# Kernel tuning notes

Hardware: AMD Instinct MI355X
Metric: run time of the kernel (lower is better)

## Reference

```python
import jax, jax.numpy as jnp
import numpy as np

DIM = 1024
HEADS = 16
HEAD_DIM = DIM // HEADS
N = 4096
EPS = 1e-5


def setup_inputs() -> dict:
    key = jax.random.key(0)
    ks = jax.random.split(key, 12)
    s = DIM ** -0.5  # init scale for weights
    return {
        "z1": jax.random.normal(ks[0], (N, DIM), jnp.float32),
        "z2": jax.random.normal(ks[1], (N, DIM), jnp.float32),
        "wq": jax.random.normal(ks[2], (DIM, DIM), jnp.float32) * s,
        "bq": jax.random.normal(ks[3], (DIM,), jnp.float32) * 0.01,
        "wk": jax.random.normal(ks[4], (DIM, DIM), jnp.float32) * s,
        "bk": jax.random.normal(ks[5], (DIM,), jnp.float32) * 0.01,
        "wv1": jax.random.normal(ks[6], (DIM, DIM), jnp.float32) * s,
        "bv1": jax.random.normal(ks[7], (DIM,), jnp.float32) * 0.01,
        "wv2": jax.random.normal(ks[8], (DIM, DIM), jnp.float32) * s,
        "bv2": jax.random.normal(ks[9], (DIM,), jnp.float32) * 0.01,
        "g1": jnp.ones((DIM,), jnp.float32),
        "be1": jnp.zeros((DIM,), jnp.float32),
        "g2": jnp.ones((DIM,), jnp.float32),
        "be2": jnp.zeros((DIM,), jnp.float32),
    }


def _layernorm(x, g, b):
    mu = jnp.mean(x, axis=-1, keepdims=True)
    var = jnp.mean(jnp.square(x - mu), axis=-1, keepdims=True)
    return (x - mu) * jax.lax.rsqrt(var + EPS) * g + b


def _split_heads(x):  # [n, dim] -> [h, n, c]
    n = x.shape[0]
    return x.reshape(n, HEADS, HEAD_DIM).swapaxes(0, 1)


def reference(z1, z2, wq, bq, wk, bk, wv1, bv1, wv2, bv2, g1, be1, g2, be2):
    scale = DIM ** -0.5
    n1 = _layernorm(z1, g1, be1)
    n2 = _layernorm(z2, g2, be2)
    q = _split_heads(n1 @ wq.T + bq)    # [h, n, c]
    k = _split_heads(n2 @ wk.T + bk)    # [h, m, c]
    v = _split_heads(n2 @ wv1.T + bv1)  # [h, m, c]
    v1 = _split_heads(n1 @ wv2.T + bv2) # [h, n, c]
    sim = jnp.einsum('hnc,hmc->hnm', q, k) * scale
    attn = jax.nn.softmax(sim, axis=-1)                       # [h, n, m]
    z_c = jnp.einsum('hnm,hmc->hnc', attn, v)                 # attn @ v
    c_z = jnp.einsum('hnm,hnc->hmc', attn, v1)                # attn.T @ v1
    z_c = z_c.swapaxes(0, 1).reshape(z1.shape[0], DIM)
    c_z = c_z.swapaxes(0, 1).reshape(z2.shape[0], DIM)
    # torch's attn.squeeze(0) is a no-op for HEADS > 1
    return z_c, c_z, attn
```

## Files before the change

kernel.cpp:

```cpp
#include <hip/hip_runtime.h>

#define NN 4096
#define DIM 1024
#define HEADS 16
#define HD 64
#define SCALE 0.03125f

typedef __attribute__((ext_vector_type(8))) short bf16x8;
typedef __attribute__((ext_vector_type(4))) short short4v;
typedef __attribute__((ext_vector_type(4))) float f32x4;
typedef __attribute__((ext_vector_type(4))) unsigned int u32x4;

__device__ __forceinline__ short f2bf(float f) {
  unsigned int x = __float_as_uint(f);
  unsigned int r = x + 0x7FFFu + ((x >> 16) & 1u);
  return (short)(r >> 16);
}
__device__ __forceinline__ unsigned int cvtpk(float a, float b) {
  unsigned int r;
  asm("v_cvt_pk_bf16_f32 %0, %1, %2" : "=v"(r) : "v"(a), "v"(b));
  return r;
}

#define GLL16(gp, lp) __builtin_amdgcn_global_load_lds( \
    (const __attribute__((address_space(1))) unsigned int*)(gp), \
    (__attribute__((address_space(3))) unsigned int*)(lp), 16, 0, 0)

#define MFMA16(a, b, c) __builtin_amdgcn_mfma_f32_16x16x32_bf16(a, b, c, 0, 0, 0)

__global__ __launch_bounds__(256) void ln_kernel(
    const float* __restrict__ z1, const float* __restrict__ z2,
    const float* __restrict__ g1, const float* __restrict__ be1,
    const float* __restrict__ g2, const float* __restrict__ be2,
    short* __restrict__ n1, short* __restrict__ n2) {
  int row = blockIdx.x;
  int which = blockIdx.y;
  const float* src = (which ? z2 : z1) + (size_t)row * DIM;
  const float* g  = which ? g2 : g1;
  const float* be = which ? be2 : be1;
  short* dst = (which ? n2 : n1) + (size_t)row * DIM;
  int t = threadIdx.x;
  float4 v = ((const float4*)src)[t];
  float s  = v.x + v.y + v.z + v.w;
  float s2 = v.x*v.x + v.y*v.y + v.z*v.z + v.w*v.w;
#pragma unroll
  for (int off = 32; off >= 1; off >>= 1) {
    s  += __shfl_xor(s, off);
    s2 += __shfl_xor(s2, off);
  }
  __shared__ __align__(16) float ls[8];
  int wid = t >> 6;
  if ((t & 63) == 0) { ls[wid] = s; ls[wid + 4] = s2; }
  __syncthreads();
  s  = ls[0] + ls[1] + ls[2] + ls[3];
  s2 = ls[4] + ls[5] + ls[6] + ls[7];
  float mu = s * (1.0f / DIM);
  float var = s2 * (1.0f / DIM) - mu * mu;
  float rs = rsqrtf(var + 1e-5f);
  float4 gv = ((const float4*)g)[t];
  float4 bv = ((const float4*)be)[t];
  short4v o;
  o.x = f2bf((v.x - mu) * rs * gv.x + bv.x);
  o.y = f2bf((v.y - mu) * rs * gv.y + bv.y);
  o.z = f2bf((v.z - mu) * rs * gv.z + bv.z);
  o.w = f2bf((v.w - mu) * rs * gv.w + bv.w);
  ((short4v*)dst)[t] = o;
}

__global__ __launch_bounds__(256) void cvt_w_kernel(
    const float* __restrict__ w0, const float* __restrict__ w1,
    const float* __restrict__ w2, const float* __restrict__ w3,
    short* __restrict__ wb) {
  int y = blockIdx.y;
  const float* src = (y == 0) ? w0 : (y == 1) ? w1 : (y == 2) ? w2 : w3;
  size_t i = (size_t)blockIdx.x * 256 + threadIdx.x;
  float4 v = ((const float4*)src)[i];
  short4v o;
  o.x = f2bf(v.x); o.y = f2bf(v.y); o.z = f2bf(v.z); o.w = f2bf(v.w);
  ((short4v*)(wb + (size_t)y * DIM * DIM))[i] = o;
}

__global__ __launch_bounds__(256) void proj_kernel(
    const short* __restrict__ n1, const short* __restrict__ n2,
    const short* __restrict__ wb,
    const float* __restrict__ bq, const float* __restrict__ bk,
    const float* __restrict__ bv1, const float* __restrict__ bv2,
    short* __restrict__ q, short* __restrict__ k,
    short* __restrict__ vT, short* __restrict__ v1T) {
  int z = blockIdx.z;
  const short* A = (z == 1 || z == 2) ? n2 : n1;
  const short* B = wb + (size_t)z * DIM * DIM;
  const float* bias = (z == 0) ? bq : (z == 1) ? bk : (z == 2) ? bv1 : bv2;
  int i0 = blockIdx.y * 128, j0 = blockIdx.x * 128;
  __shared__ __align__(16) short As[128 * 32];
  __shared__ __align__(16) short Bs[128 * 32];
  int t = threadIdx.x;
  int wid = t >> 6, lane = t & 63, g = lane >> 4, l15 = lane & 15;
  int wi = (wid >> 1) * 64, wj = (wid & 1) * 64;
  f32x4 acc[4][4] = {};
  for (int kt = 0; kt < DIM; kt += 32) {
    __syncthreads();
#pragma unroll
    for (int e = 0; e < 2; ++e) {
      int lin = e * 256 + t;
      int row = lin >> 2, kc = (lin & 3) * 8;
      GLL16(A + (size_t)(i0 + row) * DIM + kt + kc, As + lin * 8);
      GLL16(B + (size_t)(j0 + row) * DIM + kt + kc, Bs + lin * 8);
    }
    __syncthreads();
    bf16x8 af[4], bfr[4];
#pragma unroll
    for (int it = 0; it < 4; ++it)
      af[it] = *(const bf16x8*)(As + (wi + it * 16 + l15) * 32 + g * 8);
#pragma unroll
    for (int jt = 0; jt < 4; ++jt)
      bfr[jt] = *(const bf16x8*)(Bs + (wj + jt * 16 + l15) * 32 + g * 8);
#pragma unroll
    for (int it = 0; it < 4; ++it)
#pragma unroll
      for (int jt = 0; jt < 4; ++jt)
        acc[it][jt] = MFMA16(af[it], bfr[jt], acc[it][jt]);
  }
  if (z < 2) {
    short* out = (z == 0) ? q : k;
#pragma unroll
    for (int jt = 0; jt < 4; ++jt) {
      int j = j0 + wj + jt * 16 + l15;
      float bj = bias[j];
#pragma unroll
      for (int it = 0; it < 4; ++it) {
        int i = i0 + wi + it * 16 + g * 4;
#pragma unroll
        for (int r = 0; r < 4; ++r)
          out[(size_t)(i + r) * DIM + j] = f2bf(acc[it][jt][r] + bj);
      }
    }
  } else {
    short* out = (z == 2) ? vT : v1T;
#pragma unroll
    for (int jt = 0; jt < 4; ++jt) {
      int j = j0 + wj + jt * 16 + l15;
      float bj = bias[j];
#pragma unroll
      for (int it = 0; it < 4; ++it) {
        int i = i0 + wi + it * 16 + g * 4;
        short4v o;
#pragma unroll
        for (int r = 0; r < 4; ++r) o[r] = f2bf(acc[it][jt][r] + bj);
        *(short4v*)(out + (size_t)j * NN + i) = o;
      }
    }
  }
}

__global__ __launch_bounds__(256, 4) void p2zc_kernel(
    const short* __restrict__ q, const short* __restrict__ k,
    const short* __restrict__ vT, float* __restrict__ attn,
    float* __restrict__ zc, float* __restrict__ iSx) {
  int bid = (int)(blockIdx.y * gridDim.x + blockIdx.x);
  int vid = (bid & 7) * 128 + (bid >> 3);
  int h = vid >> 6;
  int nblk = vid & 63;
  int t = threadIdx.x, wid = t >> 6, lane = t & 63;
  int g = lane >> 4, l15 = lane & 15;
  int nw = nblk * 64 + wid * 16;

  const short* qp = q + (size_t)(nw + l15) * DIM + h * HD + g * 8;
  bf16x8 qb0 = *(const bf16x8*)(qp);
  bf16x8 qb1 = *(const bf16x8*)(qp + 32);

  __shared__ __align__(16) short Ks[128 * 64];
  __shared__ __align__(16) short Vs[64 * 128];
  const short* kb = k + h * HD;
  const short* vb = vT + (size_t)h * HD * NN;

  f32x4 Sp = {0.f, 0.f, 0.f, 0.f};
  for (int mc = 0; mc < NN; mc += 128) {
    __syncthreads();
#pragma unroll
    for (int e = 0; e < 4; ++e) {
      int L = e * 256 + t, row = L >> 3, c = L & 7;
      GLL16(kb + (size_t)(mc + row) * DIM + ((c ^ (row & 7)) * 8), Ks + L * 8);
    }
    __syncthreads();
#pragma unroll
    for (int mt = 0; mt < 8; ++mt) {
      const short* kr = Ks + (mt * 16 + l15) * 64;
      bf16x8 ka0 = *(const bf16x8*)(kr + ((g ^ (l15 & 7)) * 8));
      bf16x8 ka1 = *(const bf16x8*)(kr + (((g + 4) ^ (l15 & 7)) * 8));
      f32x4 acc = {0.f, 0.f, 0.f, 0.f};
      acc = MFMA16(ka0, qb0, acc);
      acc = MFMA16(ka1, qb1, acc);
#pragma unroll
      for (int r = 0; r < 4; ++r) Sp[r] += __expf(acc[r] * SCALE);
    }
  }
  float S = Sp[0] + Sp[1] + Sp[2] + Sp[3];
  S += __shfl_xor(S, 16);
  S += __shfl_xor(S, 32);
  float iS = 1.0f / S;
  if (lane < 16) iSx[h * NN + nw + l15] = iS;

  float* ab = attn + (size_t)h * NN * NN;
  f32x4 azc[4] = {};
  for (int mc = 0; mc < NN; mc += 128) {
    __syncthreads();
#pragma unroll
    for (int e = 0; e < 4; ++e) {
      int L = e * 256 + t, row = L >> 3, c = L & 7;
      GLL16(kb + (size_t)(mc + row) * DIM + ((c ^ (row & 7)) * 8), Ks + L * 8);
    }
#pragma unroll
    for (int e = 0; e < 4; ++e) {
      int L = e * 256 + t, row = L >> 4, c = L & 15;
      GLL16(vb + (size_t)row * NN + mc + ((c ^ (row & 15)) * 8), Vs + L * 8);
    }
    __syncthreads();
    float p[8][4];
#pragma unroll
    for (int mt = 0; mt < 8; ++mt) {
      const short* kr = Ks + (mt * 16 + l15) * 64;
      bf16x8 ka0 = *(const bf16x8*)(kr + ((g ^ (l15 & 7)) * 8));
      bf16x8 ka1 = *(const bf16x8*)(kr + (((g + 4) ^ (l15 & 7)) * 8));
      f32x4 acc = {0.f, 0.f, 0.f, 0.f};
      acc = MFMA16(ka0, qb0, acc);
      acc = MFMA16(ka1, qb1, acc);
      f32x4 pv;
#pragma unroll
      for (int r = 0; r < 4; ++r) { pv[r] = __expf(acc[r] * SCALE) * iS; p[mt][r] = pv[r]; }
      *(f32x4*)(ab + (size_t)(nw + l15) * NN + mc + mt * 16 + g * 4) = pv;
    }
#pragma unroll
    for (int km = 0; km < 4; ++km) {
      unsigned int a0p = cvtpk(p[2*km][0],   p[2*km][1]);
      unsigned int a1p = cvtpk(p[2*km][2],   p[2*km][3]);
      unsigned int b0p = cvtpk(p[2*km+1][0], p[2*km+1][1]);
      unsigned int b1p = cvtpk(p[2*km+1][2], p[2*km+1][3]);
      int s0 = ((g & 1) * 2) * 16 + l15, s1 = s0 + 16;
      bool hi = g >= 2;
      unsigned int w0a = __shfl(a0p, s0), w0b = __shfl(b0p, s0);
      unsigned int w1a = __shfl(a1p, s0), w1b = __shfl(b1p, s0);
      unsigned int w2a = __shfl(a0p, s1), w2b = __shfl(b0p, s1);
      unsigned int w3a = __shfl(a1p, s1), w3b = __shfl(b1p, s1);
      union { u32x4 u; bf16x8 s; } pw;
      pw.u[0] = hi ? w0b : w0a; pw.u[1] = hi ? w1b : w1a;
      pw.u[2] = hi ? w2b : w2a; pw.u[3] = hi ? w3b : w3a;
#pragma unroll
      for (int ct = 0; ct < 4; ++ct) {
        bf16x8 pb = *(const bf16x8*)(Vs + (ct * 16 + l15) * 128 + (((km * 4 + g) ^ l15) * 8));
        azc[ct] = MFMA16(pw.s, pb, azc[ct]);
      }
    }
  }
#pragma unroll
  for (int ct = 0; ct < 4; ++ct)
#pragma unroll
    for (int r = 0; r < 4; ++r)
      zc[(size_t)(nw + g * 4 + r) * DIM + h * HD + ct * 16 + l15] = azc[ct][r];
}

__global__ __launch_bounds__(256, 4) void czr_kernel(
    const short* __restrict__ q, const short* __restrict__ k,
    const short* __restrict__ v1T, const float* __restrict__ iSx,
    float* __restrict__ cz) {
  int bid = (int)(blockIdx.y * gridDim.x + blockIdx.x);
  int vid = (bid & 7) * 128 + (bid >> 3);
  int h = vid >> 6;
  int mblk = vid & 63;
  int t = threadIdx.x, wid = t >> 6, lane = t & 63;
  int g = lane >> 4, l15 = lane & 15;
  int mw = mblk * 64 + wid * 16;

  const short* kp = k + (size_t)(mw + l15) * DIM + h * HD + g * 8;
  bf16x8 kb0 = *(const bf16x8*)(kp);
  bf16x8 kb1 = *(const bf16x8*)(kp + 32);

  __shared__ __align__(16) short Qs[128 * 64];
  __shared__ __align__(16) short V1s[64 * 128];
  const short* qb = q + h * HD;
  const short* vb = v1T + (size_t)h * HD * NN;
  const float* iSb = iSx + h * NN;

  f32x4 acz[4] = {};
  for (int nc = 0; nc < NN; nc += 128) {
    __syncthreads();
#pragma unroll
    for (int e = 0; e < 4; ++e) {
      int L = e * 256 + t, row = L >> 3, c = L & 7;
      GLL16(qb + (size_t)(nc + row) * DIM + ((c ^ (row & 7)) * 8), Qs + L * 8);
    }
#pragma unroll
    for (int e = 0; e < 4; ++e) {
      int L = e * 256 + t, row = L >> 4, c = L & 15;
      GLL16(vb + (size_t)row * NN + nc + ((c ^ (row & 15)) * 8), V1s + L * 8);
    }
    __syncthreads();
    float p[8][4];
#pragma unroll
    for (int nt = 0; nt < 8; ++nt) {
      const short* qr = Qs + (nt * 16 + l15) * 64;
      bf16x8 qa0 = *(const bf16x8*)(qr + ((g ^ (l15 & 7)) * 8));
      bf16x8 qa1 = *(const bf16x8*)(qr + (((g + 4) ^ (l15 & 7)) * 8));
      f32x4 acc = {0.f, 0.f, 0.f, 0.f};
      acc = MFMA16(qa0, kb0, acc);
      acc = MFMA16(qa1, kb1, acc);
      f32x4 is4 = *(const f32x4*)(iSb + nc + nt * 16 + g * 4);
#pragma unroll
      for (int r = 0; r < 4; ++r) p[nt][r] = __expf(acc[r] * SCALE) * is4[r];
    }
#pragma unroll
    for (int kn = 0; kn < 4; ++kn) {
      unsigned int a0p = cvtpk(p[2*kn][0],   p[2*kn][1]);
      unsigned int a1p = cvtpk(p[2*kn][2],   p[2*kn][3]);
      unsigned int b0p = cvtpk(p[2*kn+1][0], p[2*kn+1][1]);
      unsigned int b1p = cvtpk(p[2*kn+1][2], p[2*kn+1][3]);
      int s0 = ((g & 1) * 2) * 16 + l15, s1 = s0 + 16;
      bool hi = g >= 2;
      unsigned int w0a = __shfl(a0p, s0), w0b = __shfl(b0p, s0);
      unsigned int w1a = __shfl(a1p, s0), w1b = __shfl(b1p, s0);
      unsigned int w2a = __shfl(a0p, s1), w2b = __shfl(b0p, s1);
      unsigned int w3a = __shfl(a1p, s1), w3b = __shfl(b1p, s1);
      union { u32x4 u; bf16x8 s; } pw;
      pw.u[0] = hi ? w0b : w0a; pw.u[1] = hi ? w1b : w1a;
      pw.u[2] = hi ? w2b : w2a; pw.u[3] = hi ? w3b : w3a;
#pragma unroll
      for (int ct = 0; ct < 4; ++ct) {
        bf16x8 pb = *(const bf16x8*)(V1s + (ct * 16 + l15) * 128 + (((kn * 4 + g) ^ l15) * 8));
        acz[ct] = MFMA16(pw.s, pb, acz[ct]);
      }
    }
  }
#pragma unroll
  for (int ct = 0; ct < 4; ++ct)
#pragma unroll
    for (int r = 0; r < 4; ++r)
      cz[(size_t)(mw + g * 4 + r) * DIM + h * HD + ct * 16 + l15] = acz[ct][r];
}

extern "C" void kernel_launch(void* const* d_in, const int* in_sizes, int n_in,
                              void* d_out, int out_size, void* d_ws, size_t ws_size,
                              hipStream_t stream) {
  static const int expect[14] = {4194304, 4194304, 1048576, 1024, 1048576, 1024,
                                 1048576, 1024, 1048576, 1024, 1024, 1024, 1024, 1024};
  if (n_in != 14) return;
  for (int i = 0; i < 14; ++i) if (in_sizes[i] != expect[i]) return;
  if (out_size != 2 * NN * DIM + (size_t)HEADS * NN * NN) return;

  const float* z1  = (const float*)d_in[0];
  const float* z2  = (const float*)d_in[1];
  const float* wq  = (const float*)d_in[2];
  const float* bq  = (const float*)d_in[3];
  const float* wk  = (const float*)d_in[4];
  const float* bk  = (const float*)d_in[5];
  const float* wv1 = (const float*)d_in[6];
  const float* bv1 = (const float*)d_in[7];
  const float* wv2 = (const float*)d_in[8];
  const float* bv2 = (const float*)d_in[9];
  const float* g1  = (const float*)d_in[10];
  const float* be1 = (const float*)d_in[11];
  const float* g2  = (const float*)d_in[12];
  const float* be2 = (const float*)d_in[13];

  float* out  = (float*)d_out;
  float* zc   = out;
  float* cz   = out + (size_t)NN * DIM;
  float* attn = out + 2 * (size_t)NN * DIM;

  short* n1 = (short*)zc;
  short* n2 = (short*)cz;
  short* wb = (short*)attn;

  char* ws = (char*)d_ws;
  const size_t MB = 1024 * 1024;
  short* q   = (short*)(ws);
  short* k   = (short*)(ws + 8 * MB);
  short* vT  = (short*)(ws + 16 * MB);
  short* v1T = (short*)(ws + 24 * MB);
  float* iSx = (float*)(ws + 32 * MB);

  ln_kernel<<<dim3(NN, 2), 256, 0, stream>>>(z1, z2, g1, be1, g2, be2, n1, n2);
  cvt_w_kernel<<<dim3(DIM * DIM / 1024, 4), 256, 0, stream>>>(wq, wk, wv1, wv2, wb);
  proj_kernel<<<dim3(DIM / 128, NN / 128, 4), 256, 0, stream>>>(n1, n2, wb, bq, bk, bv1, bv2, q, k, vT, v1T);
  p2zc_kernel<<<dim3(NN / 64, HEADS), 256, 0, stream>>>(q, k, vT, attn, zc, iSx);
  czr_kernel<<<dim3(NN / 64, HEADS), 256, 0, stream>>>(q, k, v1T, iSx, cz);
}
```

Before: 559.0 us.

## Double per-wave row tiles, use native exp2, prescale v1 by inverse row sums

Each wave now handles two 16-row tiles in the attention kernels, so each K/Q tile loaded into LDS is reused twice as often and the grid is halved. __expf is replaced by a raw v_exp_f32 on a prescaled argument. A new small kernel folds the per-row inverse softmax sums into v1T beforehand, which removes the iSx loads and multiplies from the czr inner loop. The cost is more registers and accumulators per wave, which may reduce occupancy, and a small extra bf16 rounding step on v1.

```diff
diff --git a/kernel.cpp b/kernel.cpp
--- a/kernel.cpp
+++ b/kernel.cpp
@@ -5,6 +5,7 @@
 #define HEADS 16
 #define HD 64
 #define SCALE 0.03125f
+#define EXP2S 0.04508422002778011f
 
 typedef __attribute__((ext_vector_type(8))) short bf16x8;
 typedef __attribute__((ext_vector_type(4))) short short4v;
@@ -16,9 +17,17 @@
   unsigned int r = x + 0x7FFFu + ((x >> 16) & 1u);
   return (short)(r >> 16);
 }
+__device__ __forceinline__ float bf2f(short s) {
+  return __uint_as_float(((unsigned int)(unsigned short)s) << 16);
+}
 __device__ __forceinline__ unsigned int cvtpk(float a, float b) {
   unsigned int r;
   asm("v_cvt_pk_bf16_f32 %0, %1, %2" : "=v"(r) : "v"(a), "v"(b));
+  return r;
+}
+__device__ __forceinline__ float exp2x(float x) {
+  float r;
+  asm("v_exp_f32 %0, %1" : "=v"(r) : "v"(x));
   return r;
 }
 
@@ -158,23 +167,27 @@
     const short* __restrict__ vT, float* __restrict__ attn,
     float* __restrict__ zc, float* __restrict__ iSx) {
   int bid = (int)(blockIdx.y * gridDim.x + blockIdx.x);
-  int vid = (bid & 7) * 128 + (bid >> 3);
-  int h = vid >> 6;
-  int nblk = vid & 63;
+  int vid = (bid & 7) * 64 + (bid >> 3);
+  int h = vid >> 5;
+  int base = (vid & 31) * 128;
   int t = threadIdx.x, wid = t >> 6, lane = t & 63;
   int g = lane >> 4, l15 = lane & 15;
-  int nw = nblk * 64 + wid * 16;
-
-  const short* qp = q + (size_t)(nw + l15) * DIM + h * HD + g * 8;
-  bf16x8 qb0 = *(const bf16x8*)(qp);
-  bf16x8 qb1 = *(const bf16x8*)(qp + 32);
+  int nw[2] = {base + wid * 16, base + 64 + wid * 16};
+
+  bf16x8 qb[2][2];
+#pragma unroll
+  for (int tl = 0; tl < 2; ++tl) {
+    const short* qp = q + (size_t)(nw[tl] + l15) * DIM + h * HD + g * 8;
+    qb[tl][0] = *(const bf16x8*)(qp);
+    qb[tl][1] = *(const bf16x8*)(qp + 32);
+  }
 
   __shared__ __align__(16) short Ks[128 * 64];
   __shared__ __align__(16) short Vs[64 * 128];
   const short* kb = k + h * HD;
   const short* vb = vT + (size_t)h * HD * NN;
 
-  f32x4 Sp = {0.f, 0.f, 0.f, 0.f};
+  float Sp[2][4] = {};
   for (int mc = 0; mc < NN; mc += 128) {
     __syncthreads();
 #pragma unroll
@@ -188,21 +201,28 @@
       const short* kr = Ks + (mt * 16 + l15) * 64;
       bf16x8 ka0 = *(const bf16x8*)(kr + ((g ^ (l15 & 7)) * 8));
       bf16x8 ka1 = *(const bf16x8*)(kr + (((g + 4) ^ (l15 & 7)) * 8));
-      f32x4 acc = {0.f, 0.f, 0.f, 0.f};
-      acc = MFMA16(ka0, qb0, acc);
-      acc = MFMA16(ka1, qb1, acc);
-#pragma unroll
-      for (int r = 0; r < 4; ++r) Sp[r] += __expf(acc[r] * SCALE);
-    }
-  }
-  float S = Sp[0] + Sp[1] + Sp[2] + Sp[3];
-  S += __shfl_xor(S, 16);
-  S += __shfl_xor(S, 32);
-  float iS = 1.0f / S;
-  if (lane < 16) iSx[h * NN + nw + l15] = iS;
+#pragma unroll
+      for (int tl = 0; tl < 2; ++tl) {
+        f32x4 acc = {0.f, 0.f, 0.f, 0.f};
+        acc = MFMA16(ka0, qb[tl][0], acc);
+        acc = MFMA16(ka1, qb[tl][1], acc);
+#pragma unroll
+        for (int r = 0; r < 4; ++r) Sp[tl][r] += exp2x(acc[r] * EXP2S);
+      }
+    }
+  }
+  float iS[2];
+#pragma unroll
+  for (int tl = 0; tl < 2; ++tl) {
+    float S = Sp[tl][0] + Sp[tl][1] + Sp[tl][2] + Sp[tl][3];
+    S += __shfl_xor(S, 16);
+    S += __shfl_xor(S, 32);
+    iS[tl] = 1.0f / S;
+    if (lane < 16) iSx[h * NN + nw[tl] + l15] = iS[tl];
+  }
 
   float* ab = attn + (size_t)h * NN * NN;
-  f32x4 azc[4] = {};
+  f32x4 azc[2][4] = {};
   for (int mc = 0; mc < NN; mc += 128) {
     __syncthreads();
 #pragma unroll
@@ -216,72 +236,100 @@
       GLL16(vb + (size_t)row * NN + mc + ((c ^ (row & 15)) * 8), Vs + L * 8);
     }
     __syncthreads();
-    float p[8][4];
-#pragma unroll
-    for (int mt = 0; mt < 8; ++mt) {
-      const short* kr = Ks + (mt * 16 + l15) * 64;
-      bf16x8 ka0 = *(const bf16x8*)(kr + ((g ^ (l15 & 7)) * 8));
-      bf16x8 ka1 = *(const bf16x8*)(kr + (((g + 4) ^ (l15 & 7)) * 8));
-      f32x4 acc = {0.f, 0.f, 0.f, 0.f};
-      acc = MFMA16(ka0, qb0, acc);
-      acc = MFMA16(ka1, qb1, acc);
-      f32x4 pv;
-#pragma unroll
-      for (int r = 0; r < 4; ++r) { pv[r] = __expf(acc[r] * SCALE) * iS; p[mt][r] = pv[r]; }
-      *(f32x4*)(ab + (size_t)(nw + l15) * NN + mc + mt * 16 + g * 4) = pv;
-    }
-#pragma unroll
-    for (int km = 0; km < 4; ++km) {
-      unsigned int a0p = cvtpk(p[2*km][0],   p[2*km][1]);
-      unsigned int a1p = cvtpk(p[2*km][2],   p[2*km][3]);
-      unsigned int b0p = cvtpk(p[2*km+1][0], p[2*km+1][1]);
-      unsigned int b1p = cvtpk(p[2*km+1][2], p[2*km+1][3]);
-      int s0 = ((g & 1) * 2) * 16 + l15, s1 = s0 + 16;
-      bool hi = g >= 2;
-      unsigned int w0a = __shfl(a0p, s0), w0b = __shfl(b0p, s0);
-      unsigned int w1a = __shfl(a1p, s0), w1b = __shfl(b1p, s0);
-      unsigned int w2a = __shfl(a0p, s1), w2b = __shfl(b0p, s1);
-      unsigned int w3a = __shfl(a1p, s1), w3b = __shfl(b1p, s1);
-      union { u32x4 u; bf16x8 s; } pw;
-      pw.u[0] = hi ? w0b : w0a; pw.u[1] = hi ? w1b : w1a;
-      pw.u[2] = hi ? w2b : w2a; pw.u[3] = hi ? w3b : w3a;
-#pragma unroll
-      for (int ct = 0; ct < 4; ++ct) {
-        bf16x8 pb = *(const bf16x8*)(Vs + (ct * 16 + l15) * 128 + (((km * 4 + g) ^ l15) * 8));
-        azc[ct] = MFMA16(pw.s, pb, azc[ct]);
+#pragma unroll
+    for (int tl = 0; tl < 2; ++tl) {
+      float* abr = ab + (size_t)(nw[tl] + l15) * NN + mc + g * 4;
+#pragma unroll
+      for (int km = 0; km < 4; ++km) {
+        f32x4 pv0, pv1;
+#pragma unroll
+        for (int half = 0; half < 2; ++half) {
+          int mt = 2 * km + half;
+          const short* kr = Ks + (mt * 16 + l15) * 64;
+          bf16x8 ka0 = *(const bf16x8*)(kr + ((g ^ (l15 & 7)) * 8));
+          bf16x8 ka1 = *(const bf16x8*)(kr + (((g + 4) ^ (l15 & 7)) * 8));
+          f32x4 acc = {0.f, 0.f, 0.f, 0.f};
+          acc = MFMA16(ka0, qb[tl][0], acc);
+          acc = MFMA16(ka1, qb[tl][1], acc);
+          f32x4 pv;
+#pragma unroll
+          for (int r = 0; r < 4; ++r) pv[r] = exp2x(acc[r] * EXP2S) * iS[tl];
+          *(f32x4*)(abr + mt * 16) = pv;
+          if (half == 0) pv0 = pv; else pv1 = pv;
+        }
+        unsigned int a0p = cvtpk(pv0[0], pv0[1]);
+        unsigned int a1p = cvtpk(pv0[2], pv0[3]);
+        unsigned int b0p = cvtpk(pv1[0], pv1[1]);
+        unsigned int b1p = cvtpk(pv1[2], pv1[3]);
+        int s0 = ((g & 1) * 2) * 16 + l15, s1 = s0 + 16;
+        bool hi = g >= 2;
+        unsigned int w0a = __shfl(a0p, s0), w0b = __shfl(b0p, s0);
+        unsigned int w1a = __shfl(a1p, s0), w1b = __shfl(b1p, s0);
+        unsigned int w2a = __shfl(a0p, s1), w2b = __shfl(b0p, s1);
+        unsigned int w3a = __shfl(a1p, s1), w3b = __shfl(b1p, s1);
+        union { u32x4 u; bf16x8 s; } pw;
+        pw.u[0] = hi ? w0b : w0a; pw.u[1] = hi ? w1b : w1a;
+        pw.u[2] = hi ? w2b : w2a; pw.u[3] = hi ? w3b : w3a;
+#pragma unroll
+        for (int ct = 0; ct < 4; ++ct) {
+          bf16x8 pb = *(const bf16x8*)(Vs + (ct * 16 + l15) * 128 + (((km * 4 + g) ^ l15) * 8));
+          azc[tl][ct] = MFMA16(pw.s, pb, azc[tl][ct]);
+        }
       }
     }
   }
 #pragma unroll
-  for (int ct = 0; ct < 4; ++ct)
-#pragma unroll
-    for (int r = 0; r < 4; ++r)
-      zc[(size_t)(nw + g * 4 + r) * DIM + h * HD + ct * 16 + l15] = azc[ct][r];
+  for (int tl = 0; tl < 2; ++tl)
+#pragma unroll
+    for (int ct = 0; ct < 4; ++ct)
+#pragma unroll
+      for (int r = 0; r < 4; ++r)
+        zc[(size_t)(nw[tl] + g * 4 + r) * DIM + h * HD + ct * 16 + l15] = azc[tl][ct][r];
+}
+
+__global__ __launch_bounds__(256) void v1scale_kernel(
+    short* __restrict__ v1T, const float* __restrict__ iSx) {
+  int row = blockIdx.y;
+  int h = row >> 6;
+  int n0 = (int)(blockIdx.x * 2048) + threadIdx.x * 8;
+  short* p = v1T + (size_t)row * NN + n0;
+  bf16x8 v = *(const bf16x8*)p;
+  const float* isb = iSx + h * NN + n0;
+  f32x4 i0 = ((const f32x4*)isb)[0];
+  f32x4 i1 = ((const f32x4*)isb)[1];
+  union { u32x4 u; bf16x8 s; } o;
+  o.u[0] = cvtpk(bf2f(v[0]) * i0[0], bf2f(v[1]) * i0[1]);
+  o.u[1] = cvtpk(bf2f(v[2]) * i0[2], bf2f(v[3]) * i0[3]);
+  o.u[2] = cvtpk(bf2f(v[4]) * i1[0], bf2f(v[5]) * i1[1]);
+  o.u[3] = cvtpk(bf2f(v[6]) * i1[2], bf2f(v[7]) * i1[3]);
+  *(bf16x8*)p = o.s;
 }
 
 __global__ __launch_bounds__(256, 4) void czr_kernel(
     const short* __restrict__ q, const short* __restrict__ k,
-    const short* __restrict__ v1T, const float* __restrict__ iSx,
-    float* __restrict__ cz) {
+    const short* __restrict__ v1T, float* __restrict__ cz) {
   int bid = (int)(blockIdx.y * gridDim.x + blockIdx.x);
-  int vid = (bid & 7) * 128 + (bid >> 3);
-  int h = vid >> 6;
-  int mblk = vid & 63;
+  int vid = (bid & 7) * 64 + (bid >> 3);
+  int h = vid >> 5;
+  int base = (vid & 31) * 128;
   int t = threadIdx.x, wid = t >> 6, lane = t & 63;
   int g = lane >> 4, l15 = lane & 15;
-  int mw = mblk * 64 + wid * 16;
-
-  const short* kp = k + (size_t)(mw + l15) * DIM + h * HD + g * 8;
-  bf16x8 kb0 = *(const bf16x8*)(kp);
-  bf16x8 kb1 = *(const bf16x8*)(kp + 32);
+  int mw[2] = {base + wid * 16, base + 64 + wid * 16};
+
+  bf16x8 kb[2][2];
+#pragma unroll
+  for (int tl = 0; tl < 2; ++tl) {
+    const short* kp = k + (size_t)(mw[tl] + l15) * DIM + h * HD + g * 8;
+    kb[tl][0] = *(const bf16x8*)(kp);
+    kb[tl][1] = *(const bf16x8*)(kp + 32);
+  }
 
   __shared__ __align__(16) short Qs[128 * 64];
   __shared__ __align__(16) short V1s[64 * 128];
   const short* qb = q + h * HD;
   const short* vb = v1T + (size_t)h * HD * NN;
-  const float* iSb = iSx + h * NN;
-
-  f32x4 acz[4] = {};
+
+  f32x4 acz[2][4] = {};
   for (int nc = 0; nc < NN; nc += 128) {
     __syncthreads();
 #pragma unroll
@@ -295,46 +343,53 @@
       GLL16(vb + (size_t)row * NN + nc + ((c ^ (row & 15)) * 8), V1s + L * 8);
     }
     __syncthreads();
-    float p[8][4];
-#pragma unroll
-    for (int nt = 0; nt < 8; ++nt) {
-      const short* qr = Qs + (nt * 16 + l15) * 64;
-      bf16x8 qa0 = *(const bf16x8*)(qr + ((g ^ (l15 & 7)) * 8));
-      bf16x8 qa1 = *(const bf16x8*)(qr + (((g + 4) ^ (l15 & 7)) * 8));
-      f32x4 acc = {0.f, 0.f, 0.f, 0.f};
-      acc = MFMA16(qa0, kb0, acc);
-      acc = MFMA16(qa1, kb1, acc);
-      f32x4 is4 = *(const f32x4*)(iSb + nc + nt * 16 + g * 4);
-#pragma unroll
-      for (int r = 0; r < 4; ++r) p[nt][r] = __expf(acc[r] * SCALE) * is4[r];
-    }
-#pragma unroll
-    for (int kn = 0; kn < 4; ++kn) {
-      unsigned int a0p = cvtpk(p[2*kn][0],   p[2*kn][1]);
-      unsigned int a1p = cvtpk(p[2*kn][2],   p[2*kn][3]);
-      unsigned int b0p = cvtpk(p[2*kn+1][0], p[2*kn+1][1]);
-      unsigned int b1p = cvtpk(p[2*kn+1][2], p[2*kn+1][3]);
-      int s0 = ((g & 1) * 2) * 16 + l15, s1 = s0 + 16;
-      bool hi = g >= 2;
-      unsigned int w0a = __shfl(a0p, s0), w0b = __shfl(b0p, s0);
-      unsigned int w1a = __shfl(a1p, s0), w1b = __shfl(b1p, s0);
-      unsigned int w2a = __shfl(a0p, s1), w2b = __shfl(b0p, s1);
-      unsigned int w3a = __shfl(a1p, s1), w3b = __shfl(b1p, s1);
-      union { u32x4 u; bf16x8 s; } pw;
-      pw.u[0] = hi ? w0b : w0a; pw.u[1] = hi ? w1b : w1a;
-      pw.u[2] = hi ? w2b : w2a; pw.u[3] = hi ? w3b : w3a;
-#pragma unroll
-      for (int ct = 0; ct < 4; ++ct) {
-        bf16x8 pb = *(const bf16x8*)(V1s + (ct * 16 + l15) * 128 + (((kn * 4 + g) ^ l15) * 8));
-        acz[ct] = MFMA16(pw.s, pb, acz[ct]);
+#pragma unroll
+    for (int tl = 0; tl < 2; ++tl) {
+#pragma unroll
+      for (int kn = 0; kn < 4; ++kn) {
+        f32x4 p0, p1;
+#pragma unroll
+        for (int half = 0; half < 2; ++half) {
+          int nt = 2 * kn + half;
+          const short* qr = Qs + (nt * 16 + l15) * 64;
+          bf16x8 qa0 = *(const bf16x8*)(qr + ((g ^ (l15 & 7)) * 8));
+          bf16x8 qa1 = *(const bf16x8*)(qr + (((g + 4) ^ (l15 & 7)) * 8));
+          f32x4 acc = {0.f, 0.f, 0.f, 0.f};
+          acc = MFMA16(qa0, kb[tl][0], acc);
+          acc = MFMA16(qa1, kb[tl][1], acc);
+          f32x4 pe;
+#pragma unroll
+          for (int r = 0; r < 4; ++r) pe[r] = exp2x(acc[r] * EXP2S);
+          if (half == 0) p0 = pe; else p1 = pe;
+        }
+        unsigned int a0p = cvtpk(p0[0], p0[1]);
+        unsigned int a1p = cvtpk(p0[2], p0[3]);
+        unsigned int b0p = cvtpk(p1[0], p1[1]);
+        unsigned int b1p = cvtpk(p1[2], p1[3]);
+        int s0 = ((g & 1) * 2) * 16 + l15, s1 = s0 + 16;
+        bool hi = g >= 2;
+        unsigned int w0a = __shfl(a0p, s0), w0b = __shfl(b0p, s0);
+        unsigned int w1a = __shfl(a1p, s0), w1b = __shfl(b1p, s0);
+        unsigned int w2a = __shfl(a0p, s1), w2b = __shfl(b0p, s1);
+        unsigned int w3a = __shfl(a1p, s1), w3b = __shfl(b1p, s1);
+        union { u32x4 u; bf16x8 s; } pw;
+        pw.u[0] = hi ? w0b : w0a; pw.u[1] = hi ? w1b : w1a;
+        pw.u[2] = hi ? w2b : w2a; pw.u[3] = hi ? w3b : w3a;
+#pragma unroll
+        for (int ct = 0; ct < 4; ++ct) {
+          bf16x8 pb = *(const bf16x8*)(V1s + (ct * 16 + l15) * 128 + (((kn * 4 + g) ^ l15) * 8));
+          acz[tl][ct] = MFMA16(pw.s, pb, acz[tl][ct]);
+        }
       }
     }
   }
 #pragma unroll
-  for (int ct = 0; ct < 4; ++ct)
-#pragma unroll
-    for (int r = 0; r < 4; ++r)
-      cz[(size_t)(mw + g * 4 + r) * DIM + h * HD + ct * 16 + l15] = acz[ct][r];
+  for (int tl = 0; tl < 2; ++tl)
+#pragma unroll
+    for (int ct = 0; ct < 4; ++ct)
+#pragma unroll
+      for (int r = 0; r < 4; ++r)
+        cz[(size_t)(mw[tl] + g * 4 + r) * DIM + h * HD + ct * 16 + l15] = acz[tl][ct][r];
 }
 
 extern "C" void kernel_launch(void* const* d_in, const int* in_sizes, int n_in,
@@ -381,6 +436,7 @@
   ln_kernel<<<dim3(NN, 2), 256, 0, stream>>>(z1, z2, g1, be1, g2, be2, n1, n2);
   cvt_w_kernel<<<dim3(DIM * DIM / 1024, 4), 256, 0, stream>>>(wq, wk, wv1, wv2, wb);
   proj_kernel<<<dim3(DIM / 128, NN / 128, 4), 256, 0, stream>>>(n1, n2, wb, bq, bk, bv1, bv2, q, k, vT, v1T);
-  p2zc_kernel<<<dim3(NN / 64, HEADS), 256, 0, stream>>>(q, k, vT, attn, zc, iSx);
-  czr_kernel<<<dim3(NN / 64, HEADS), 256, 0, stream>>>(q, k, v1T, iSx, cz);
-}
+  p2zc_kernel<<<dim3(NN / 128, HEADS), 256, 0, stream>>>(q, k, vT, attn, zc, iSx);
+  v1scale_kernel<<<dim3(NN / 2048, DIM), 256, 0, stream>>>(v1T, iSx);
+  czr_kernel<<<dim3(NN / 128, HEADS), 256, 0, stream>>>(q, k, v1T, cz);
+}
```

Result: slower. 602.6 us (+7.8%).

## Fold softmax row normalizer into V1 and use native exp2

Applied to the files above, without the earlier changes.

Replaces __expf with the raw v_exp_f32 instruction on a pre-scaled argument (scale times log2 e) in both attention kernels. It also moves the per-row 1/S normalization out of the cz kernel's inner loop: a new small kernel multiplies v1T by iSx in place before czr runs. This removes the per-tile iSx loads and multiplies from the hot loop, at the cost of an extra pass over v1T and an extra bf16 rounding of the scaled values.

```diff
diff --git a/kernel.cpp b/kernel.cpp
--- a/kernel.cpp
+++ b/kernel.cpp
@@ -5,6 +5,7 @@
 #define HEADS 16
 #define HD 64
 #define SCALE 0.03125f
+#define EXP2S 0.04508422002778011f
 
 typedef __attribute__((ext_vector_type(8))) short bf16x8;
 typedef __attribute__((ext_vector_type(4))) short short4v;
@@ -16,9 +17,17 @@
   unsigned int r = x + 0x7FFFu + ((x >> 16) & 1u);
   return (short)(r >> 16);
 }
+__device__ __forceinline__ float bf2f(short s) {
+  return __uint_as_float(((unsigned int)(unsigned short)s) << 16);
+}
 __device__ __forceinline__ unsigned int cvtpk(float a, float b) {
   unsigned int r;
   asm("v_cvt_pk_bf16_f32 %0, %1, %2" : "=v"(r) : "v"(a), "v"(b));
+  return r;
+}
+__device__ __forceinline__ float exp2x(float x) {
+  float r;
+  asm("v_exp_f32 %0, %1" : "=v"(r) : "v"(x));
   return r;
 }
 
@@ -192,7 +201,7 @@
       acc = MFMA16(ka0, qb0, acc);
       acc = MFMA16(ka1, qb1, acc);
 #pragma unroll
-      for (int r = 0; r < 4; ++r) Sp[r] += __expf(acc[r] * SCALE);
+      for (int r = 0; r < 4; ++r) Sp[r] += exp2x(acc[r] * EXP2S);
     }
   }
   float S = Sp[0] + Sp[1] + Sp[2] + Sp[3];
@@ -227,7 +236,7 @@
       acc = MFMA16(ka1, qb1, acc);
       f32x4 pv;
 #pragma unroll
-      for (int r = 0; r < 4; ++r) { pv[r] = __expf(acc[r] * SCALE) * iS; p[mt][r] = pv[r]; }
+      for (int r = 0; r < 4; ++r) { pv[r] = exp2x(acc[r] * EXP2S) * iS; p[mt][r] = pv[r]; }
       *(f32x4*)(ab + (size_t)(nw + l15) * NN + mc + mt * 16 + g * 4) = pv;
     }
 #pragma unroll
@@ -259,10 +268,27 @@
       zc[(size_t)(nw + g * 4 + r) * DIM + h * HD + ct * 16 + l15] = azc[ct][r];
 }
 
+__global__ __launch_bounds__(256) void v1scale_kernel(
+    short* __restrict__ v1T, const float* __restrict__ iSx) {
+  int row = blockIdx.y;
+  int h = row >> 6;
+  int n0 = (int)(blockIdx.x * 2048) + threadIdx.x * 8;
+  short* p = v1T + (size_t)row * NN + n0;
+  bf16x8 v = *(const bf16x8*)p;
+  const float* isb = iSx + h * NN + n0;
+  f32x4 i0 = ((const f32x4*)isb)[0];
+  f32x4 i1 = ((const f32x4*)isb)[1];
+  union { u32x4 u; bf16x8 s; } o;
+  o.u[0] = cvtpk(bf2f(v[0]) * i0[0], bf2f(v[1]) * i0[1]);
+  o.u[1] = cvtpk(bf2f(v[2]) * i0[2], bf2f(v[3]) * i0[3]);
+  o.u[2] = cvtpk(bf2f(v[4]) * i1[0], bf2f(v[5]) * i1[1]);
+  o.u[3] = cvtpk(bf2f(v[6]) * i1[2], bf2f(v[7]) * i1[3]);
+  *(bf16x8*)p = o.s;
+}
+
 __global__ __launch_bounds__(256, 4) void czr_kernel(
     const short* __restrict__ q, const short* __restrict__ k,
-    const short* __restrict__ v1T, const float* __restrict__ iSx,
-    float* __restrict__ cz) {
+    const short* __restrict__ v1T, float* __restrict__ cz) {
   int bid = (int)(blockIdx.y * gridDim.x + blockIdx.x);
   int vid = (bid & 7) * 128 + (bid >> 3);
   int h = vid >> 6;
@@ -279,7 +305,6 @@
   __shared__ __align__(16) short V1s[64 * 128];
   const short* qb = q + h * HD;
   const short* vb = v1T + (size_t)h * HD * NN;
-  const float* iSb = iSx + h * NN;
 
   f32x4 acz[4] = {};
   for (int nc = 0; nc < NN; nc += 128) {
@@ -304,9 +329,8 @@
       f32x4 acc = {0.f, 0.f, 0.f, 0.f};
       acc = MFMA16(qa0, kb0, acc);
       acc = MFMA16(qa1, kb1, acc);
-      f32x4 is4 = *(const f32x4*)(iSb + nc + nt * 16 + g * 4);
-#pragma unroll
-      for (int r = 0; r < 4; ++r) p[nt][r] = __expf(acc[r] * SCALE) * is4[r];
+#pragma unroll
+      for (int r = 0; r < 4; ++r) p[nt][r] = exp2x(acc[r] * EXP2S);
     }
 #pragma unroll
     for (int kn = 0; kn < 4; ++kn) {
@@ -382,5 +406,6 @@
   cvt_w_kernel<<<dim3(DIM * DIM / 1024, 4), 256, 0, stream>>>(wq, wk, wv1, wv2, wb);
   proj_kernel<<<dim3(DIM / 128, NN / 128, 4), 256, 0, stream>>>(n1, n2, wb, bq, bk, bv1, bv2, q, k, vT, v1T);
   p2zc_kernel<<<dim3(NN / 64, HEADS), 256, 0, stream>>>(q, k, vT, attn, zc, iSx);
-  czr_kernel<<<dim3(NN / 64, HEADS), 256, 0, stream>>>(q, k, v1T, iSx, cz);
-}
+  v1scale_kernel<<<dim3(NN / 2048, DIM), 256, 0, stream>>>(v1T, iSx);
+  czr_kernel<<<dim3(NN / 64, HEADS), 256, 0, stream>>>(q, k, v1T, cz);
+}
```

Measured after the change: 535.2 us. -4.3%, faster.
